# Kernel tuning notes

Measured on AMD Instinct MI355X. Metric: run time of the kernel, lower is better.

Reference implementation:

```python
import jax, jax.numpy as jnp
import numpy as np
import math

C = 512
TEXT_DIM = 768
HEADS = 8
HEAD_DIM = C // HEADS
GROUPS = 32
EPS = 1e-5


def setup_inputs() -> dict:
    key = jax.random.key(0)
    ks = jax.random.split(key, 12)
    B, H, W, T = 16, 64, 64, 77
    s = lambda fan_in: 1.0 / math.sqrt(fan_in)
    return {
        "x": jax.random.normal(ks[0], (B, C, H, W), jnp.float32),
        "text_emb": jax.random.normal(ks[1], (B, T, TEXT_DIM), jnp.float32),
        "gn_gamma": jnp.ones((C,), jnp.float32),
        "gn_beta": jnp.zeros((C,), jnp.float32),
        "q_w": jax.random.uniform(ks[2], (C, C), jnp.float32, -s(C), s(C)),
        "q_b": jax.random.uniform(ks[3], (C,), jnp.float32, -s(C), s(C)),
        "k_w": jax.random.uniform(ks[4], (C, TEXT_DIM), jnp.float32, -s(TEXT_DIM), s(TEXT_DIM)),
        "k_b": jax.random.uniform(ks[5], (C,), jnp.float32, -s(TEXT_DIM), s(TEXT_DIM)),
        "v_w": jax.random.uniform(ks[6], (C, TEXT_DIM), jnp.float32, -s(TEXT_DIM), s(TEXT_DIM)),
        "v_b": jax.random.uniform(ks[7], (C,), jnp.float32, -s(TEXT_DIM), s(TEXT_DIM)),
        "proj_w": jax.random.uniform(ks[8], (C, C), jnp.float32, -s(C), s(C)),
        "proj_b": jax.random.uniform(ks[9], (C,), jnp.float32, -s(C), s(C)),
    }


def _group_norm(x, gamma, beta):
    b, c, h, w = x.shape
    xg = x.reshape(b, GROUPS, c // GROUPS, h, w)
    mu = jnp.mean(xg, axis=(2, 3, 4), keepdims=True)
    var = jnp.var(xg, axis=(2, 3, 4), keepdims=True)
    xg = (xg - mu) * jax.lax.rsqrt(var + EPS)
    return xg.reshape(b, c, h, w) * gamma[None, :, None, None] + beta[None, :, None, None]


def reference(x, text_emb, gn_gamma, gn_beta, q_w, q_b, k_w, k_b, v_w, v_b, proj_w, proj_b):
    b, c, h, w = x.shape
    residual = x
    xn = _group_norm(x, gn_gamma, gn_beta)
    # 1x1 conv Q: [b,c,h,w] -> [b,c,h,w]
    q = jnp.einsum('bchw,oc->bohw', xn, q_w) + q_b[None, :, None, None]
    q = q.reshape(b, HEADS, HEAD_DIM, h * w)                  # [b,hd,dh,hw]
    # K,V linear then RAW reshape (matches torch's view semantics exactly)
    k = (jnp.einsum('btf,cf->btc', text_emb, k_w) + k_b).reshape(b, HEADS, HEAD_DIM, -1)
    v = (jnp.einsum('btf,cf->btc', text_emb, v_w) + v_b).reshape(b, HEADS, HEAD_DIM, -1)
    scale = 1.0 / math.sqrt(HEAD_DIM)
    attn = jax.nn.softmax(jnp.einsum('bhds,bhdt->bhst', q, k) * scale, axis=-1)
    out = jnp.einsum('bhst,bhdt->bhds', attn, v)              # [b,hd,dh,hw]
    out = out.reshape(b, c, h, w)
    out = jnp.einsum('bchw,oc->bohw', out, proj_w) + proj_b[None, :, None, None]
    return out + residual
```

## Files before the change

kernel.cpp:

```cpp
#include <hip/hip_runtime.h>

typedef unsigned short USHORT;
typedef __attribute__((ext_vector_type(8))) short short8;
typedef __attribute__((ext_vector_type(4))) float f32x4;

#define NB   16
#define NC   512
#define NHW  4096
#define NT   77
#define NF   768
#define NHEAD 8
#define NDH  64
#define TPAD 80
#define TPAD2 96
#define PSTR 104
#define BKS  64

__device__ __forceinline__ USHORT f2bf(float f){
  unsigned u = __builtin_bit_cast(unsigned, f);
  u += 0x7fffu + ((u >> 16) & 1u);
  return (USHORT)(u >> 16);
}
__device__ __forceinline__ unsigned pack2(float a, float b){
  return (unsigned)f2bf(a) | ((unsigned)f2bf(b) << 16);
}

__device__ __forceinline__ void gload16(const void* g, void* l){
  __builtin_amdgcn_global_load_lds((const __attribute__((address_space(1))) unsigned*)g,
                                   (__attribute__((address_space(3))) unsigned*)l, 16, 0, 0);
}

__device__ __forceinline__ int xcd_swz32(int x){ return ((x & 7) << 2) | (x >> 3); }

__global__ __launch_bounds__(256) void cvt_all_kernel(const float* __restrict__ s0, USHORT* __restrict__ d0, int n0,
                                                      const float* __restrict__ s1, USHORT* __restrict__ d1, int n1,
                                                      const float* __restrict__ s2, USHORT* __restrict__ d2, int n2,
                                                      const float* __restrict__ s3, USHORT* __restrict__ d3, int n3,
                                                      const float* __restrict__ s4, USHORT* __restrict__ d4, int n4){
  int i = blockIdx.x * 256 + threadIdx.x;
  const float* s; USHORT* d;
  if (i < n0){ s = s0; d = d0; }
  else { i -= n0;
    if (i < n1){ s = s1; d = d1; }
    else { i -= n1;
      if (i < n2){ s = s2; d = d2; }
      else { i -= n2;
        if (i < n3){ s = s3; d = d3; }
        else { i -= n3;
          if (i >= n4) return;
          s = s4; d = d4; } } } }
  float4 v = ((const float4*)s)[i];
  uint2 pk; pk.x = pack2(v.x, v.y); pk.y = pack2(v.z, v.w);
  ((uint2*)d)[i] = pk;
}

__global__ __launch_bounds__(256) void gnstats_kernel(const float* __restrict__ x, float2* __restrict__ stats){
  int gid = blockIdx.x;
  const float4* p = (const float4*)(x + (size_t)gid * 65536);
  float s = 0.f, s2 = 0.f;
  for (int i = threadIdx.x; i < 16384; i += 256){
    float4 v = p[i];
    s  += v.x + v.y + v.z + v.w;
    s2 += v.x*v.x + v.y*v.y + v.z*v.z + v.w*v.w;
  }
  #pragma unroll
  for (int off = 32; off; off >>= 1){ s += __shfl_down(s, off); s2 += __shfl_down(s2, off); }
  __shared__ float red[8];
  int wv = threadIdx.x >> 6;
  if ((threadIdx.x & 63) == 0){ red[wv] = s; red[4 + wv] = s2; }
  __syncthreads();
  if (threadIdx.x == 0){
    float S  = red[0] + red[1] + red[2] + red[3];
    float S2 = red[4] + red[5] + red[6] + red[7];
    float mu = S * (1.0f / 65536.0f);
    float var = S2 * (1.0f / 65536.0f) - mu * mu;
    stats[gid] = make_float2(mu, 1.0f / sqrtf(var + 1e-5f));
  }
}

__global__ __launch_bounds__(256) void gnorm_tr_kernel(const float* __restrict__ x, const float2* __restrict__ stats,
                                                       const float* __restrict__ gamma, const float* __restrict__ beta,
                                                       USHORT* __restrict__ xnT){
  __shared__ float tile[64][65];
  int b = blockIdx.z, c0 = blockIdx.y * 64, s0 = blockIdx.x * 64;
  int col = threadIdx.x & 63;
  int row4 = threadIdx.x >> 6;
  const float* xp = x + ((size_t)b * NC + c0) * NHW + s0;
  #pragma unroll
  for (int i = 0; i < 16; i++){
    int r = i * 4 + row4;
    tile[r][col] = xp[(size_t)r * NHW + col];
  }
  __syncthreads();
  int c = c0 + col;
  int g = c >> 4;
  float2 st = stats[b * 32 + g];
  float ga = gamma[c], be = beta[c];
  USHORT* op = xnT + ((size_t)b * NHW + s0) * NC + c;
  #pragma unroll
  for (int i = 0; i < 16; i++){
    int s = i * 4 + row4;
    float v = (tile[col][s] - st.x) * st.y * ga + be;
    op[(size_t)s * NC] = f2bf(v);
  }
}

__device__ __forceinline__ void gemm128_core(const USHORT* __restrict__ A, const USHORT* __restrict__ B,
                                             int m0, size_t brow0, USHORT* Alds, USHORT* Blds,
                                             f32x4 (&acc)[4][4]){
  const int tid = threadIdx.x;
  const int lane = tid & 63, wave = tid >> 6;
  const int l15 = lane & 15, lg = lane >> 4;
  const int wm = wave >> 1, wn = wave & 1;
  const int srow = lane >> 3, sslot = lane & 7;

  #pragma unroll
  for (int i = 0; i < 4; i++)
    #pragma unroll
    for (int j = 0; j < 4; j++) acc[i][j] = f32x4{0.f, 0.f, 0.f, 0.f};

  for (int k0 = 0; k0 < 512; k0 += BKS){
    #pragma unroll
    for (int i = 0; i < 4; i++){
      const int r0 = wave * 32 + i * 8;
      const int row = r0 + srow;
      const int slot = sslot ^ (row & 7);
      gload16(A + (size_t)(m0 + row) * NC + k0 + slot * 8, Alds + r0 * BKS);
      gload16(B + brow0 + (size_t)row * NC + k0 + slot * 8, Blds + r0 * BKS);
    }
    __syncthreads();
    #pragma unroll
    for (int ks = 0; ks < 2; ks++){
      short8 af[4], bf[4];
      #pragma unroll
      for (int i = 0; i < 4; i++){
        const int row = wm * 64 + i * 16 + l15;
        af[i] = *(const short8*)(Alds + row * BKS + (((ks * 4 + lg) ^ (row & 7)) * 8));
      }
      #pragma unroll
      for (int j = 0; j < 4; j++){
        const int row = wn * 64 + j * 16 + l15;
        bf[j] = *(const short8*)(Blds + row * BKS + (((ks * 4 + lg) ^ (row & 7)) * 8));
      }
      #pragma unroll
      for (int i = 0; i < 4; i++)
        #pragma unroll
        for (int j = 0; j < 4; j++)
          acc[i][j] = __builtin_amdgcn_mfma_f32_16x16x32_bf16(af[i], bf[j], acc[i][j], 0, 0, 0);
    }
    __syncthreads();
  }
}

__global__ __launch_bounds__(256, 3) void qattn_kernel(const USHORT* __restrict__ Aw, const USHORT* __restrict__ Bx,
                                                       const float* __restrict__ bias,
                                                       const USHORT* __restrict__ kb, const USHORT* __restrict__ vb,
                                                       USHORT* __restrict__ attnT){
  __shared__ USHORT smem[26624];
  const int lane = threadIdx.x & 63, wave = threadIdx.x >> 6;
  const int l15 = lane & 15, lg = lane >> 4;
  const int b = blockIdx.z;
  const int xx = xcd_swz32(blockIdx.x);
  const int m0b = blockIdx.y * 128;
  const size_t brow0 = ((size_t)b * NHW + xx * 128) * NC;
  f32x4 acc[4][4];
  gemm128_core(Aw, Bx, m0b, brow0, smem, smem + 8192, acc);

  const int wm = wave >> 1, wn = wave & 1;
  const int h = blockIdx.y * 2 + wm;
  const int m0 = h * 64;
  const int s0 = xx * 128 + wn * 64;
  const size_t bh = (size_t)b * NHEAD + h;
  char* qt = (char*)(smem + wave * 6656);

  #pragma unroll
  for (int i = 0; i < 4; i++){
    const int dbase = i * 16 + lg * 4;
    float b0 = bias[m0 + dbase], b1 = bias[m0 + dbase + 1];
    float b2 = bias[m0 + dbase + 2], b3 = bias[m0 + dbase + 3];
    #pragma unroll
    for (int j = 0; j < 4; j++){
      const int s = j * 16 + l15;
      uint2 pk;
      pk.x = pack2(acc[i][j][0] + b0, acc[i][j][1] + b1);
      pk.y = pack2(acc[i][j][2] + b2, acc[i][j][3] + b3);
      *(uint2*)(qt + s * 128 + ((dbase * 2) ^ ((s & 7) << 4))) = pk;
    }
  }
  short8 aq[4][2];
  #pragma unroll
  for (int i = 0; i < 4; i++){
    const int s = i * 16 + l15;
    #pragma unroll
    for (int ks = 0; ks < 2; ks++)
      aq[i][ks] = *(const short8*)(qt + s * 128 + ((ks * 64 + lg * 16) ^ ((s & 7) << 4)));
  }

  USHORT* plds = (USHORT*)qt;
  uint4 z{0u, 0u, 0u, 0u};
  *(uint4*)(qt + lane * (PSTR * 2) + 160) = z;
  *(uint4*)(qt + lane * (PSTR * 2) + 176) = z;

  short8 bk[5][2];
  const USHORT* kp = kb + bh * TPAD * NDH;
  #pragma unroll
  for (int j = 0; j < 5; j++)
    #pragma unroll
    for (int ks = 0; ks < 2; ks++)
      bk[j][ks] = *(const short8*)(kp + (j * 16 + l15) * NDH + ks * 32 + lg * 8);

  f32x4 sacc[4][5];
  #pragma unroll
  for (int i = 0; i < 4; i++)
    #pragma unroll
    for (int j = 0; j < 5; j++) sacc[i][j] = f32x4{0.f, 0.f, 0.f, 0.f};
  #pragma unroll
  for (int ks = 0; ks < 2; ks++)
    #pragma unroll
    for (int i = 0; i < 4; i++)
      #pragma unroll
      for (int j = 0; j < 5; j++)
        sacc[i][j] = __builtin_amdgcn_mfma_f32_16x16x32_bf16(aq[i][ks], bk[j][ks], sacc[i][j], 0, 0, 0);

  const float scale = 0.125f;
  #pragma unroll
  for (int i = 0; i < 4; i++){
    float v[5][4], mx[4], sm[4];
    #pragma unroll
    for (int r = 0; r < 4; r++) mx[r] = -3.0e38f;
    #pragma unroll
    for (int j = 0; j < 5; j++)
      #pragma unroll
      for (int r = 0; r < 4; r++){
        float t = sacc[i][j][r] * scale;
        if (j == 4 && l15 >= 13) t = -3.0e38f;
        v[j][r] = t;
        mx[r] = fmaxf(mx[r], t);
      }
    #pragma unroll
    for (int r = 0; r < 4; r++)
      #pragma unroll
      for (int d = 1; d < 16; d <<= 1) mx[r] = fmaxf(mx[r], __shfl_xor(mx[r], d));
    #pragma unroll
    for (int r = 0; r < 4; r++) sm[r] = 0.f;
    #pragma unroll
    for (int j = 0; j < 5; j++)
      #pragma unroll
      for (int r = 0; r < 4; r++){
        float p = __expf(v[j][r] - mx[r]);
        v[j][r] = p;
        sm[r] += p;
      }
    #pragma unroll
    for (int r = 0; r < 4; r++)
      #pragma unroll
      for (int d = 1; d < 16; d <<= 1) sm[r] += __shfl_xor(sm[r], d);
    #pragma unroll
    for (int r = 0; r < 4; r++){
      float inv = 1.0f / sm[r];
      #pragma unroll
      for (int j = 0; j < 5; j++)
        plds[(i * 16 + lg * 4 + r) * PSTR + j * 16 + l15] = f2bf(v[j][r] * inv);
    }
  }

  f32x4 oacc[4][4];
  #pragma unroll
  for (int it = 0; it < 4; it++)
    #pragma unroll
    for (int jt = 0; jt < 4; jt++) oacc[it][jt] = f32x4{0.f, 0.f, 0.f, 0.f};
  const USHORT* vp = vb + bh * NDH * TPAD2;
  #pragma unroll
  for (int ks = 0; ks < 3; ks++){
    short8 av[4], bpv[4];
    #pragma unroll
    for (int it = 0; it < 4; it++)
      av[it] = *(const short8*)(vp + (it * 16 + l15) * TPAD2 + ks * 32 + lg * 8);
    #pragma unroll
    for (int jt = 0; jt < 4; jt++)
      bpv[jt] = *(const short8*)(plds + (jt * 16 + l15) * PSTR + ks * 32 + lg * 8);
    #pragma unroll
    for (int it = 0; it < 4; it++)
      #pragma unroll
      for (int jt = 0; jt < 4; jt++)
        oacc[it][jt] = __builtin_amdgcn_mfma_f32_16x16x32_bf16(av[it], bpv[jt], oacc[it][jt], 0, 0, 0);
  }

  USHORT* ob = attnT + ((size_t)b * NHW + s0) * NC + h * NDH;
  #pragma unroll
  for (int it = 0; it < 4; it++)
    #pragma unroll
    for (int jt = 0; jt < 4; jt++){
      const int sl = jt * 16 + l15;
      uint2 pk;
      pk.x = pack2(oacc[it][jt][0], oacc[it][jt][1]);
      pk.y = pack2(oacc[it][jt][2], oacc[it][jt][3]);
      *(uint2*)(ob + (size_t)sl * NC + it * 16 + lg * 4) = pk;
    }
}

__global__ __launch_bounds__(256, 3) void projgemm_kernel(const USHORT* __restrict__ Aw, const USHORT* __restrict__ Battn,
                                                          const float* __restrict__ bias, const float* __restrict__ xres,
                                                          float* __restrict__ out){
  __shared__ USHORT Alds[128 * BKS], Blds[128 * BKS];
  const int b = blockIdx.z;
  const int xx = xcd_swz32(blockIdx.x);
  const int m0b = blockIdx.y * 128;
  const size_t brow0 = ((size_t)b * NHW + xx * 128) * NC;
  f32x4 acc[4][4];
  gemm128_core(Aw, Battn, m0b, brow0, Alds, Blds, acc);

  const int lane = threadIdx.x & 63, wave = threadIdx.x >> 6;
  const int l15 = lane & 15, lg = lane >> 4;
  const int m0 = m0b + (wave >> 1) * 64;
  const int n0 = xx * 128 + (wave & 1) * 64;
  #pragma unroll
  for (int i = 0; i < 4; i++){
    const int ob = m0 + i * 16 + lg * 4;
    #pragma unroll
    for (int r = 0; r < 4; r++){
      const int oc = ob + r;
      const float bb = bias[oc];
      #pragma unroll
      for (int j = 0; j < 4; j++){
        const int s = n0 + j * 16 + l15;
        const size_t idx = ((size_t)b * NC + oc) * NHW + s;
        out[idx] = acc[i][j][r] + bb + xres[idx];
      }
    }
  }
}

template<int KLEN>
__device__ __forceinline__ void mfma_core(const USHORT* const (&ap)[4], const USHORT* const (&bp)[4],
                                          f32x4 (&acc)[4][4]){
  short8 a_c[4], b_c[4];
  #pragma unroll
  for (int i = 0; i < 4; i++){ a_c[i] = *(const short8*)ap[i]; b_c[i] = *(const short8*)bp[i]; }
  #pragma unroll 2
  for (int k0 = 0; k0 < KLEN; k0 += 32){
    short8 a_n[4], b_n[4];
    if (k0 + 32 < KLEN){
      #pragma unroll
      for (int i = 0; i < 4; i++){
        a_n[i] = *(const short8*)(ap[i] + k0 + 32);
        b_n[i] = *(const short8*)(bp[i] + k0 + 32);
      }
    }
    #pragma unroll
    for (int i = 0; i < 4; i++)
      #pragma unroll
      for (int j = 0; j < 4; j++)
        acc[i][j] = __builtin_amdgcn_mfma_f32_16x16x32_bf16(a_c[i], b_c[j], acc[i][j], 0, 0, 0);
    #pragma unroll
    for (int i = 0; i < 4; i++){ a_c[i] = a_n[i]; b_c[i] = b_n[i]; }
  }
}

__global__ __launch_bounds__(256, 2) void kvgemm_kernel(const USHORT* __restrict__ kw, const USHORT* __restrict__ vw,
                                                        const USHORT* __restrict__ Tx,
                                                        const float* __restrict__ kbias, const float* __restrict__ vbias,
                                                        USHORT* __restrict__ kdst, USHORT* __restrict__ vdst){
  const int lane = threadIdx.x & 63, wave = threadIdx.x >> 6;
  const int l15 = lane & 15, lg = lane >> 4;
  const int b = blockIdx.z;
  const int mode = blockIdx.y;
  const USHORT* Wt = mode ? vw : kw;
  const float* bias = mode ? vbias : kbias;
  USHORT* dst = mode ? vdst : kdst;
  const int m0 = (wave >> 1) * 64;
  const int n0 = blockIdx.x * 128 + (wave & 1) * 64;
  const USHORT* ap[4]; const USHORT* bp[4];
  #pragma unroll
  for (int i = 0; i < 4; i++){
    int r = m0 + i * 16 + l15; r = r > 76 ? 76 : r;
    ap[i] = Tx + ((size_t)b * NT + r) * NF + lg * 8;
  }
  #pragma unroll
  for (int i = 0; i < 4; i++) bp[i] = Wt + (size_t)(n0 + i * 16 + l15) * NF + lg * 8;
  f32x4 acc[4][4];
  #pragma unroll
  for (int i = 0; i < 4; i++)
    #pragma unroll
    for (int j = 0; j < 4; j++) acc[i][j] = f32x4{0.f, 0.f, 0.f, 0.f};
  mfma_core<NF>(ap, bp, acc);
  #pragma unroll
  for (int i = 0; i < 4; i++){
    const int tb = m0 + i * 16 + lg * 4;
    #pragma unroll
    for (int r = 0; r < 4; r++){
      const int t = tb + r;
      if (t < NT){
        #pragma unroll
        for (int j = 0; j < 4; j++){
          const int c = n0 + j * 16 + l15;
          float v = acc[i][j][r] + bias[c];
          int fi = t * NC + c;
          int hh = fi / 4928;
          int rem = fi - hh * 4928;
          int dd = rem / 77;
          int tt = rem - dd * 77;
          size_t bhh = (size_t)(b * NHEAD + hh);
          if (mode == 0) dst[(bhh * TPAD + tt) * NDH + dd] = f2bf(v);
          else           dst[(bhh * NDH + dd) * TPAD2 + tt] = f2bf(v);
        }
      }
    }
  }
}

extern "C" void kernel_launch(void* const* d_in, const int* in_sizes, int n_in,
                              void* d_out, int out_size, void* d_ws, size_t ws_size,
                              hipStream_t stream){
  const float* x    = (const float*)d_in[0];
  const float* text = (const float*)d_in[1];
  const float* gn_g = (const float*)d_in[2];
  const float* gn_b = (const float*)d_in[3];
  const float* q_w  = (const float*)d_in[4];
  const float* q_b  = (const float*)d_in[5];
  const float* k_w  = (const float*)d_in[6];
  const float* k_b  = (const float*)d_in[7];
  const float* v_w  = (const float*)d_in[8];
  const float* v_b  = (const float*)d_in[9];
  const float* p_w  = (const float*)d_in[10];
  const float* p_b  = (const float*)d_in[11];
  float* out = (float*)d_out;

  char* ws = (char*)d_ws;
  size_t off = 0;
  auto alloc = [&](size_t bytes){ size_t o = off; off = (off + bytes + 255) & ~(size_t)255; return o; };
  size_t o_stats = alloc(512 * 8);
  size_t o_qwb   = alloc((size_t)NC * NC * 2);
  size_t o_pwb   = alloc((size_t)NC * NC * 2);
  size_t o_kwb   = alloc((size_t)NC * NF * 2);
  size_t o_vwb   = alloc((size_t)NC * NF * 2);
  size_t o_txb   = alloc((size_t)NB * NT * NF * 2);
  size_t o_kb    = alloc((size_t)NB * NHEAD * TPAD * NDH * 2);
  size_t o_vb    = alloc((size_t)NB * NHEAD * NDH * TPAD2 * 2);
  size_t o_xnT   = alloc((size_t)NB * NHW * NC * 2);
  size_t o_attnT = alloc((size_t)NB * NHW * NC * 2);
  (void)ws_size; (void)in_sizes; (void)n_in; (void)out_size;

  float2* stats = (float2*)(ws + o_stats);
  USHORT* qwb = (USHORT*)(ws + o_qwb);
  USHORT* pwb = (USHORT*)(ws + o_pwb);
  USHORT* kwb = (USHORT*)(ws + o_kwb);
  USHORT* vwb = (USHORT*)(ws + o_vwb);
  USHORT* txb = (USHORT*)(ws + o_txb);
  USHORT* kbuf = (USHORT*)(ws + o_kb);
  USHORT* vbuf = (USHORT*)(ws + o_vb);
  USHORT* xnT = (USHORT*)(ws + o_xnT);
  USHORT* attnT = (USHORT*)(ws + o_attnT);

  const int n0 = (NC * NC) / 4, n1 = (NC * NC) / 4, n2 = (NC * NF) / 4, n3 = (NC * NF) / 4,
            n4 = (NB * NT * NF) / 4;
  const int ntot = n0 + n1 + n2 + n3 + n4;
  hipLaunchKernelGGL(cvt_all_kernel, dim3((ntot + 255) / 256), dim3(256), 0, stream,
                     q_w, qwb, n0, p_w, pwb, n1, k_w, kwb, n2, v_w, vwb, n3, text, txb, n4);

  hipLaunchKernelGGL(gnstats_kernel, dim3(512), dim3(256), 0, stream, x, stats);
  hipLaunchKernelGGL(gnorm_tr_kernel, dim3(64, 8, 16), dim3(256), 0, stream, x, stats, gn_g, gn_b, xnT);
  hipLaunchKernelGGL(kvgemm_kernel, dim3(4, 2, 16), dim3(256), 0, stream, kwb, vwb, txb, k_b, v_b, kbuf, vbuf);
  hipLaunchKernelGGL(qattn_kernel, dim3(32, 4, 16), dim3(256), 0, stream, qwb, xnT, q_b, kbuf, vbuf, attnT);
  hipLaunchKernelGGL(projgemm_kernel, dim3(32, 4, 16), dim3(256), 0, stream, pwb, attnT, p_b, x, out);
}
```

Measured before the change: 259.8 us.

## Use 256x256-tile double-buffered projection GEMM with 512 threads

Adds a new projection GEMM kernel with 256x256 output tiles, 8 waves and 128KB of dynamic LDS, double-buffering the K loop so global loads overlap MFMA work. The larger tile is meant to raise operand reuse and cut global traffic relative to the 128x128 tile. It falls back to the old kernel if the shared-memory attribute cannot be set. The cost is 128KB of LDS per block, which lowers occupancy, and only 512 blocks are launched, which may leave some CUs underused.

```diff
diff --git a/kernel.cpp b/kernel.cpp
--- a/kernel.cpp
+++ b/kernel.cpp
@@ -31,6 +31,7 @@
 }
 
 __device__ __forceinline__ int xcd_swz32(int x){ return ((x & 7) << 2) | (x >> 3); }
+__device__ __forceinline__ int xcd_swz16(int x){ return ((x & 7) << 1) | (x >> 3); }
 
 __global__ __launch_bounds__(256) void cvt_all_kernel(const float* __restrict__ s0, USHORT* __restrict__ d0, int n0,
                                                       const float* __restrict__ s1, USHORT* __restrict__ d1, int n1,
@@ -299,6 +300,88 @@
     }
 }
 
+__global__ __launch_bounds__(512, 2) void projgemm256_kernel(const USHORT* __restrict__ Aw, const USHORT* __restrict__ Battn,
+                                                             const float* __restrict__ bias, const float* __restrict__ xres,
+                                                             float* __restrict__ out){
+  extern __shared__ __align__(16) USHORT lds[];
+  const int tid = threadIdx.x;
+  const int lane = tid & 63, wave = tid >> 6;
+  const int l15 = lane & 15, lg = lane >> 4;
+  const int wm = wave >> 2, wn = wave & 3;
+  const int b = blockIdx.z;
+  const int m0b = blockIdx.y * 256;
+  const int xx = xcd_swz16(blockIdx.x);
+  const int n0 = xx * 256;
+  const size_t brow0 = ((size_t)b * NHW + n0) * NC;
+
+  f32x4 acc[8][4];
+  #pragma unroll
+  for (int i = 0; i < 8; i++)
+    #pragma unroll
+    for (int j = 0; j < 4; j++) acc[i][j] = f32x4{0.f, 0.f, 0.f, 0.f};
+
+  auto stage = [&](int k0, int buf){
+    USHORT* Ad = lds + buf * 32768;
+    USHORT* Bd = Ad + 16384;
+    #pragma unroll
+    for (int i = 0; i < 4; i++){
+      const int rb = i * 64 + wave * 8;
+      const int row = rb + (lane >> 3);
+      const int slot = (lane & 7) ^ (row & 7);
+      gload16(Aw + (size_t)(m0b + row) * NC + k0 + slot * 8, Ad + rb * BKS);
+      gload16(Battn + brow0 + (size_t)row * NC + k0 + slot * 8, Bd + rb * BKS);
+    }
+  };
+
+  stage(0, 0);
+  __syncthreads();
+  int cur = 0;
+  for (int t = 0; t < 8; ++t){
+    if (t < 7) stage((t + 1) * BKS, cur ^ 1);
+    const USHORT* Ab = lds + cur * 32768;
+    const USHORT* Bb = Ab + 16384;
+    #pragma unroll
+    for (int ks = 0; ks < 2; ks++){
+      short8 af[8], bf[4];
+      #pragma unroll
+      for (int i = 0; i < 8; i++){
+        const int row = wm * 128 + i * 16 + l15;
+        af[i] = *(const short8*)(Ab + row * BKS + (((ks * 4 + lg) ^ (row & 7)) * 8));
+      }
+      #pragma unroll
+      for (int j = 0; j < 4; j++){
+        const int row = wn * 64 + j * 16 + l15;
+        bf[j] = *(const short8*)(Bb + row * BKS + (((ks * 4 + lg) ^ (row & 7)) * 8));
+      }
+      __builtin_amdgcn_s_setprio(1);
+      #pragma unroll
+      for (int i = 0; i < 8; i++)
+        #pragma unroll
+        for (int j = 0; j < 4; j++)
+          acc[i][j] = __builtin_amdgcn_mfma_f32_16x16x32_bf16(af[i], bf[j], acc[i][j], 0, 0, 0);
+      __builtin_amdgcn_s_setprio(0);
+    }
+    __syncthreads();
+    cur ^= 1;
+  }
+
+  #pragma unroll
+  for (int i = 0; i < 8; i++){
+    const int ob = m0b + wm * 128 + i * 16 + lg * 4;
+    #pragma unroll
+    for (int r = 0; r < 4; r++){
+      const int oc = ob + r;
+      const float bb = bias[oc];
+      #pragma unroll
+      for (int j = 0; j < 4; j++){
+        const int s = n0 + wn * 64 + j * 16 + l15;
+        const size_t idx = ((size_t)b * NC + oc) * NHW + s;
+        out[idx] = acc[i][j][r] + bb + xres[idx];
+      }
+    }
+  }
+}
+
 __global__ __launch_bounds__(256, 3) void projgemm_kernel(const USHORT* __restrict__ Aw, const USHORT* __restrict__ Battn,
                                                           const float* __restrict__ bias, const float* __restrict__ xres,
                                                           float* __restrict__ out){
@@ -462,5 +545,13 @@
   hipLaunchKernelGGL(gnorm_tr_kernel, dim3(64, 8, 16), dim3(256), 0, stream, x, stats, gn_g, gn_b, xnT);
   hipLaunchKernelGGL(kvgemm_kernel, dim3(4, 2, 16), dim3(256), 0, stream, kwb, vwb, txb, k_b, v_b, kbuf, vbuf);
   hipLaunchKernelGGL(qattn_kernel, dim3(32, 4, 16), dim3(256), 0, stream, qwb, xnT, q_b, kbuf, vbuf, attnT);
-  hipLaunchKernelGGL(projgemm_kernel, dim3(32, 4, 16), dim3(256), 0, stream, pwb, attnT, p_b, x, out);
-}
+
+  hipError_t e = hipFuncSetAttribute((const void*)projgemm256_kernel,
+                                     hipFuncAttributeMaxDynamicSharedMemorySize, 131072);
+  if (e == hipSuccess){
+    hipLaunchKernelGGL(projgemm256_kernel, dim3(16, 2, 16), dim3(512), 131072, stream,
+                       pwb, attnT, p_b, x, out);
+  } else {
+    hipLaunchKernelGGL(projgemm_kernel, dim3(32, 4, 16), dim3(256), 0, stream, pwb, attnT, p_b, x, out);
+  }
+}
```

New measurement: 261.9 us. No clear change (+0.8%).

## Fuse group-norm statistics and normalize-transpose into one register-resident kernel

Applied to the files above, without the earlier changes.

Replaces the separate GroupNorm stats kernel and the tiled normalize/transpose kernel with a single kernel. Each 512-thread block holds one (batch, group) slab of 16 channels by 4096 pixels in registers, reduces mean and variance, then writes normalized bf16 output transposed with 16-byte stores. This removes the second full read of x and one launch, and drops the stats buffer. The cost is heavy register use (128 floats per thread) and only 512 blocks. The block index is also permuted to spread work across XCDs.

```diff
diff --git a/kernel.cpp b/kernel.cpp
--- a/kernel.cpp
+++ b/kernel.cpp
@@ -54,54 +54,62 @@
   ((uint2*)d)[i] = pk;
 }
 
-__global__ __launch_bounds__(256) void gnstats_kernel(const float* __restrict__ x, float2* __restrict__ stats){
-  int gid = blockIdx.x;
-  const float4* p = (const float4*)(x + (size_t)gid * 65536);
+__global__ __launch_bounds__(512, 2) void gn_fused_kernel(const float* __restrict__ x,
+                                                          const float* __restrict__ gamma,
+                                                          const float* __restrict__ beta,
+                                                          USHORT* __restrict__ xnT){
+  const int dsp = blockIdx.x;
+  const int o = (dsp >> 3) & 1;
+  const int p = (dsp >> 4) * 8 + (dsp & 7);
+  const int base = 2 * p + o;
+  const int b = base >> 5, g = base & 31;
+  const int t = threadIdx.x;
+
+  const float* xg = x + ((size_t)b * NC + g * 16) * NHW + t * 8;
+  float vv[16][8];
   float s = 0.f, s2 = 0.f;
-  for (int i = threadIdx.x; i < 16384; i += 256){
-    float4 v = p[i];
-    s  += v.x + v.y + v.z + v.w;
-    s2 += v.x*v.x + v.y*v.y + v.z*v.z + v.w*v.w;
+  #pragma unroll
+  for (int c = 0; c < 16; c++){
+    *(float4*)&vv[c][0] = *(const float4*)(xg + (size_t)c * NHW);
+    *(float4*)&vv[c][4] = *(const float4*)(xg + (size_t)c * NHW + 4);
+    #pragma unroll
+    for (int e = 0; e < 8; e++){ s += vv[c][e]; s2 += vv[c][e] * vv[c][e]; }
   }
   #pragma unroll
   for (int off = 32; off; off >>= 1){ s += __shfl_down(s, off); s2 += __shfl_down(s2, off); }
-  __shared__ float red[8];
-  int wv = threadIdx.x >> 6;
-  if ((threadIdx.x & 63) == 0){ red[wv] = s; red[4 + wv] = s2; }
+  __shared__ float red[18];
+  const int wv = t >> 6;
+  if ((t & 63) == 0){ red[wv] = s; red[8 + wv] = s2; }
   __syncthreads();
-  if (threadIdx.x == 0){
-    float S  = red[0] + red[1] + red[2] + red[3];
-    float S2 = red[4] + red[5] + red[6] + red[7];
+  if (t == 0){
+    float S = 0.f, S2 = 0.f;
+    #pragma unroll
+    for (int i = 0; i < 8; i++){ S += red[i]; S2 += red[8 + i]; }
     float mu = S * (1.0f / 65536.0f);
     float var = S2 * (1.0f / 65536.0f) - mu * mu;
-    stats[gid] = make_float2(mu, 1.0f / sqrtf(var + 1e-5f));
-  }
-}
-
-__global__ __launch_bounds__(256) void gnorm_tr_kernel(const float* __restrict__ x, const float2* __restrict__ stats,
-                                                       const float* __restrict__ gamma, const float* __restrict__ beta,
-                                                       USHORT* __restrict__ xnT){
-  __shared__ float tile[64][65];
-  int b = blockIdx.z, c0 = blockIdx.y * 64, s0 = blockIdx.x * 64;
-  int col = threadIdx.x & 63;
-  int row4 = threadIdx.x >> 6;
-  const float* xp = x + ((size_t)b * NC + c0) * NHW + s0;
-  #pragma unroll
-  for (int i = 0; i < 16; i++){
-    int r = i * 4 + row4;
-    tile[r][col] = xp[(size_t)r * NHW + col];
+    red[16] = mu;
+    red[17] = 1.0f / sqrtf(var + 1e-5f);
   }
   __syncthreads();
-  int c = c0 + col;
-  int g = c >> 4;
-  float2 st = stats[b * 32 + g];
-  float ga = gamma[c], be = beta[c];
-  USHORT* op = xnT + ((size_t)b * NHW + s0) * NC + c;
-  #pragma unroll
-  for (int i = 0; i < 16; i++){
-    int s = i * 4 + row4;
-    float v = (tile[col][s] - st.x) * st.y * ga + be;
-    op[(size_t)s * NC] = f2bf(v);
+  const float mu = red[16], rs = red[17];
+
+  float ga[16], be[16];
+  #pragma unroll
+  for (int c = 0; c < 16; c++){ ga[c] = gamma[g * 16 + c] * rs; be[c] = beta[g * 16 + c]; }
+
+  USHORT* ob = xnT + ((size_t)b * NHW + t * 8) * NC + g * 16;
+  #pragma unroll
+  for (int e = 0; e < 8; e++){
+    unsigned w[8];
+    #pragma unroll
+    for (int c2 = 0; c2 < 8; c2++){
+      float a0 = (vv[2 * c2][e]     - mu) * ga[2 * c2]     + be[2 * c2];
+      float a1 = (vv[2 * c2 + 1][e] - mu) * ga[2 * c2 + 1] + be[2 * c2 + 1];
+      w[c2] = pack2(a0, a1);
+    }
+    uint4 p0{w[0], w[1], w[2], w[3]}, p1{w[4], w[5], w[6], w[7]};
+    *(uint4*)(ob + (size_t)e * NC) = p0;
+    *(uint4*)(ob + (size_t)e * NC + 8) = p1;
   }
 }
 
@@ -429,7 +437,6 @@
   char* ws = (char*)d_ws;
   size_t off = 0;
   auto alloc = [&](size_t bytes){ size_t o = off; off = (off + bytes + 255) & ~(size_t)255; return o; };
-  size_t o_stats = alloc(512 * 8);
   size_t o_qwb   = alloc((size_t)NC * NC * 2);
   size_t o_pwb   = alloc((size_t)NC * NC * 2);
   size_t o_kwb   = alloc((size_t)NC * NF * 2);
@@ -441,7 +448,6 @@
   size_t o_attnT = alloc((size_t)NB * NHW * NC * 2);
   (void)ws_size; (void)in_sizes; (void)n_in; (void)out_size;
 
-  float2* stats = (float2*)(ws + o_stats);
   USHORT* qwb = (USHORT*)(ws + o_qwb);
   USHORT* pwb = (USHORT*)(ws + o_pwb);
   USHORT* kwb = (USHORT*)(ws + o_kwb);
@@ -458,8 +464,7 @@
   hipLaunchKernelGGL(cvt_all_kernel, dim3((ntot + 255) / 256), dim3(256), 0, stream,
                      q_w, qwb, n0, p_w, pwb, n1, k_w, kwb, n2, v_w, vwb, n3, text, txb, n4);
 
-  hipLaunchKernelGGL(gnstats_kernel, dim3(512), dim3(256), 0, stream, x, stats);
-  hipLaunchKernelGGL(gnorm_tr_kernel, dim3(64, 8, 16), dim3(256), 0, stream, x, stats, gn_g, gn_b, xnT);
+  hipLaunchKernelGGL(gn_fused_kernel, dim3(512), dim3(512), 0, stream, x, gn_g, gn_b, xnT);
   hipLaunchKernelGGL(kvgemm_kernel, dim3(4, 2, 16), dim3(256), 0, stream, kwb, vwb, txb, k_b, v_b, kbuf, vbuf);
   hipLaunchKernelGGL(qattn_kernel, dim3(32, 4, 16), dim3(256), 0, stream, qwb, xnT, q_b, kbuf, vbuf, attnT);
   hipLaunchKernelGGL(projgemm_kernel, dim3(32, 4, 16), dim3(256), 0, stream, pwb, attnT, p_b, x, out);
```

Result: faster. 244.4 us (-5.9%).

## Fuse group-norm statistics and normalize-transpose into one LDS-staged kernel

Applied to the files above, without the earlier changes.

Replaces the separate group-norm statistics kernel and the normalize/transpose kernel with a single kernel, one 1024-thread block per (batch, group). The block reads its 16 channels of x once, accumulates sum and sum-of-squares, and stages the values as bf16 in 128 KB of dynamic LDS, then writes normalized bf16 in channel-last layout. This removes the second full pass over the large fp32 input and one launch. In exchange, x is rounded to bf16 before normalization (double rounding), occupancy is limited to one block per CU by the LDS footprint, and the old path is kept as a fallback if the shared-memory attribute cannot be set.

```diff
diff --git a/kernel.cpp b/kernel.cpp
--- a/kernel.cpp
+++ b/kernel.cpp
@@ -23,6 +23,9 @@
 }
 __device__ __forceinline__ unsigned pack2(float a, float b){
   return (unsigned)f2bf(a) | ((unsigned)f2bf(b) << 16);
+}
+__device__ __forceinline__ float bf2f(unsigned hs){
+  return __builtin_bit_cast(float, hs << 16);
 }
 
 __device__ __forceinline__ void gload16(const void* g, void* l){
@@ -54,6 +57,76 @@
   ((uint2*)d)[i] = pk;
 }
 
+__global__ __launch_bounds__(1024) void gn_fused_kernel(const float* __restrict__ x,
+                                                        const float* __restrict__ gamma,
+                                                        const float* __restrict__ beta,
+                                                        USHORT* __restrict__ xnT){
+  extern __shared__ USHORT tile[];
+  __shared__ float red[34];
+  const int dsp = blockIdx.x;
+  const int o = (dsp >> 3) & 1;
+  const int p = (dsp >> 4) * 8 + (dsp & 7);
+  const int base = 2 * p + o;
+  const int b = base >> 5, g = base & 31;
+  const int t = threadIdx.x;
+
+  const float* xg = x + ((size_t)b * NC + g * 16) * NHW + t * 4;
+  float s = 0.f, s2 = 0.f;
+  #pragma unroll
+  for (int c = 0; c < 16; c++){
+    float4 v = *(const float4*)(xg + (size_t)c * NHW);
+    s  += v.x + v.y + v.z + v.w;
+    s2 += v.x*v.x + v.y*v.y + v.z*v.z + v.w*v.w;
+    uint2 pk; pk.x = pack2(v.x, v.y); pk.y = pack2(v.z, v.w);
+    *(uint2*)(tile + c * 4096 + t * 4) = pk;
+  }
+
+  #pragma unroll
+  for (int off = 32; off; off >>= 1){ s += __shfl_down(s, off); s2 += __shfl_down(s2, off); }
+  const int wv = t >> 6;
+  if ((t & 63) == 0){ red[wv] = s; red[16 + wv] = s2; }
+  __syncthreads();
+  if (t == 0){
+    float S = 0.f, S2 = 0.f;
+    #pragma unroll
+    for (int i = 0; i < 16; i++){ S += red[i]; S2 += red[16 + i]; }
+    float mu = S * (1.0f / 65536.0f);
+    float var = S2 * (1.0f / 65536.0f) - mu * mu;
+    red[32] = mu;
+    red[33] = 1.0f / sqrtf(var + 1e-5f);
+  }
+  __syncthreads();
+  const float mu = red[32], rs = red[33];
+
+  float ga[16], be[16];
+  #pragma unroll
+  for (int c = 0; c < 16; c++){ ga[c] = gamma[g * 16 + c] * rs; be[c] = beta[g * 16 + c]; }
+
+#define GN_RD(c) uint2 u##c = *(const uint2*)(tile + (c) * 4096 + t * 4);
+  GN_RD(0)  GN_RD(1)  GN_RD(2)  GN_RD(3)  GN_RD(4)  GN_RD(5)  GN_RD(6)  GN_RD(7)
+  GN_RD(8)  GN_RD(9)  GN_RD(10) GN_RD(11) GN_RD(12) GN_RD(13) GN_RD(14) GN_RD(15)
+#undef GN_RD
+
+  USHORT* ob = xnT + ((size_t)b * NHW + t * 4) * NC + g * 16;
+#define GN_VAL(c, W, HI) bf2f(HI ? (u##c.W >> 16) : (u##c.W & 0xffffu))
+#define GN_STORE(W, HI, EIDX) { \
+  unsigned w0 = pack2((GN_VAL(0,W,HI)  - mu) * ga[0]  + be[0],  (GN_VAL(1,W,HI)  - mu) * ga[1]  + be[1]);  \
+  unsigned w1 = pack2((GN_VAL(2,W,HI)  - mu) * ga[2]  + be[2],  (GN_VAL(3,W,HI)  - mu) * ga[3]  + be[3]);  \
+  unsigned w2 = pack2((GN_VAL(4,W,HI)  - mu) * ga[4]  + be[4],  (GN_VAL(5,W,HI)  - mu) * ga[5]  + be[5]);  \
+  unsigned w3 = pack2((GN_VAL(6,W,HI)  - mu) * ga[6]  + be[6],  (GN_VAL(7,W,HI)  - mu) * ga[7]  + be[7]);  \
+  unsigned w4 = pack2((GN_VAL(8,W,HI)  - mu) * ga[8]  + be[8],  (GN_VAL(9,W,HI)  - mu) * ga[9]  + be[9]);  \
+  unsigned w5 = pack2((GN_VAL(10,W,HI) - mu) * ga[10] + be[10], (GN_VAL(11,W,HI) - mu) * ga[11] + be[11]); \
+  unsigned w6 = pack2((GN_VAL(12,W,HI) - mu) * ga[12] + be[12], (GN_VAL(13,W,HI) - mu) * ga[13] + be[13]); \
+  unsigned w7 = pack2((GN_VAL(14,W,HI) - mu) * ga[14] + be[14], (GN_VAL(15,W,HI) - mu) * ga[15] + be[15]); \
+  uint4 p0{w0, w1, w2, w3}, p1{w4, w5, w6, w7};  \
+  *(uint4*)(ob + (size_t)(EIDX) * NC) = p0;      \
+  *(uint4*)(ob + (size_t)(EIDX) * NC + 8) = p1;  \
+}
+  GN_STORE(x, 0, 0) GN_STORE(x, 1, 1) GN_STORE(y, 0, 2) GN_STORE(y, 1, 3)
+#undef GN_STORE
+#undef GN_VAL
+}
+
 __global__ __launch_bounds__(256) void gnstats_kernel(const float* __restrict__ x, float2* __restrict__ stats){
   int gid = blockIdx.x;
   const float4* p = (const float4*)(x + (size_t)gid * 65536);
@@ -458,8 +531,14 @@
   hipLaunchKernelGGL(cvt_all_kernel, dim3((ntot + 255) / 256), dim3(256), 0, stream,
                      q_w, qwb, n0, p_w, pwb, n1, k_w, kwb, n2, v_w, vwb, n3, text, txb, n4);
 
-  hipLaunchKernelGGL(gnstats_kernel, dim3(512), dim3(256), 0, stream, x, stats);
-  hipLaunchKernelGGL(gnorm_tr_kernel, dim3(64, 8, 16), dim3(256), 0, stream, x, stats, gn_g, gn_b, xnT);
+  hipError_t e = hipFuncSetAttribute((const void*)gn_fused_kernel,
+                                     hipFuncAttributeMaxDynamicSharedMemorySize, 131072);
+  if (e == hipSuccess){
+    hipLaunchKernelGGL(gn_fused_kernel, dim3(512), dim3(1024), 131072, stream, x, gn_g, gn_b, xnT);
+  } else {
+    hipLaunchKernelGGL(gnstats_kernel, dim3(512), dim3(256), 0, stream, x, stats);
+    hipLaunchKernelGGL(gnorm_tr_kernel, dim3(64, 8, 16), dim3(256), 0, stream, x, stats, gn_g, gn_b, xnT);
+  }
   hipLaunchKernelGGL(kvgemm_kernel, dim3(4, 2, 16), dim3(256), 0, stream, kwb, vwb, txb, k_b, v_b, kbuf, vbuf);
   hipLaunchKernelGGL(qattn_kernel, dim3(32, 4, 16), dim3(256), 0, stream, qwb, xnT, q_b, kbuf, vbuf, attnT);
   hipLaunchKernelGGL(projgemm_kernel, dim3(32, 4, 16), dim3(256), 0, stream, pwb, attnT, p_b, x, out);
```

Measured after the change: 241.1 us, median of 3. 1.08x faster.
